# Performance work log

Hardware: AMD Instinct MI355X
Metric: run time of the kernel (lower is better)

Reference implementation:

```python
import jax, jax.numpy as jnp
import numpy as np

B_, L_, H_, P_ = 8, 4096, 512, 256
DT_LO, DT_HI = 1e-3, 4e-3  # keep Heinsen log-space weights in fp32 range for L=4096


def setup_inputs() -> dict:
    key = jax.random.key(0)
    ks = jax.random.split(key, 8)
    u = jax.random.normal(ks[0], (B_, L_, H_), dtype=jnp.float32)
    # Diagonal continuous-time state matrix Lambda (HiPPO-N-like: Re=-0.5, structured imag parts)
    lambda_re = -0.5 * jnp.ones((P_,), dtype=jnp.float32)
    lambda_im = jnp.pi * (jnp.arange(P_, dtype=jnp.float32) + 1.0)
    # Input/output projections (complex, stored as re/im pairs)
    B_re = jax.random.normal(ks[1], (P_, H_), dtype=jnp.float32) / jnp.sqrt(float(H_))
    B_im = jax.random.normal(ks[2], (P_, H_), dtype=jnp.float32) / jnp.sqrt(float(H_))
    C_re = jax.random.normal(ks[3], (H_, P_), dtype=jnp.float32) / jnp.sqrt(float(P_))
    C_im = jax.random.normal(ks[4], (H_, P_), dtype=jnp.float32) / jnp.sqrt(float(P_))
    D = jax.random.normal(ks[5], (H_,), dtype=jnp.float32)
    # Per-state learnable log-timescales, log-uniform in [DT_LO, DT_HI]
    log_delta = jax.random.uniform(ks[6], (P_,), dtype=jnp.float32,
                                   minval=jnp.log(DT_LO), maxval=jnp.log(DT_HI))
    return {"u": u, "lambda_re": lambda_re, "lambda_im": lambda_im,
            "B_re": B_re, "B_im": B_im, "C_re": C_re, "C_im": C_im,
            "D": D, "log_delta": log_delta}


def reference(u, lambda_re, lambda_im, B_re, B_im, C_re, C_im, D, log_delta):
    # --- ZOH discretization (eq. 6 of S5 paper) ---
    lam = lambda_re + 1j * lambda_im                     # (P,) complex64
    delta = jnp.exp(log_delta)                           # (P,)
    lambda_bar = jnp.exp(lam * delta)                    # (P,) complex
    B_tilde = B_re + 1j * B_im                           # (P,H)
    B_bar = ((lambda_bar - 1.0) / lam)[:, None] * B_tilde  # (P,H)

    # --- input projection: Bu_k = B_bar @ u_k ---
    Bu = jnp.einsum('blh,ph->blp', u.astype(B_bar.dtype), B_bar)  # (B,L,P) complex

    # --- Heinsen log-space parallel scan: x_k = lambda_bar * x_{k-1} + Bu_k ---
    L = u.shape[1]
    log_lambda = jnp.log(lambda_bar)                     # (P,) complex
    k = jnp.arange(L, dtype=jnp.float32)
    weights = jnp.exp(k[:, None] * log_lambda[None, :])  # (L,P) complex
    xs = weights[None] * jnp.cumsum(Bu / weights[None], axis=1)  # (B,L,P)

    # --- output: y_k = 2*Re(C_tilde x_k) + D*u_k (conjugate symmetry) ---
    C_tilde = C_re + 1j * C_im                           # (H,P)
    y = 2.0 * jnp.real(jnp.einsum('blp,hp->blh', xs, C_tilde)) + D * u
    return y
```

## Files before the change

kernel.cpp:

```cpp
#include <hip/hip_runtime.h>
#include <hip/hip_bf16.h>
#include <math.h>

#define HH 512
#define PP 256
#define LSEQ 4096
#define BB 8
#define MTOT (BB*LSEQ)
#define N2P 512

typedef __attribute__((ext_vector_type(8))) short bf16x8;
typedef __attribute__((ext_vector_type(4))) float f32x4;
typedef __attribute__((ext_vector_type(8))) unsigned short u16x8;
typedef __attribute__((ext_vector_type(4))) unsigned short u16x4;

#define SWZ(row) (((((row) & 7) ^ (((row) >> 3) & 7)) << 4))

__device__ inline unsigned short f2b(float x) {
    return __builtin_bit_cast(unsigned short, __float2bfloat16(x));
}
__device__ inline float b2f(unsigned short h) {
    union { unsigned int u; float f; } v; v.u = ((unsigned int)h) << 16;
    return v.f;
}

#define GLOAD16(gp, lp) __builtin_amdgcn_global_load_lds( \
    (const __attribute__((address_space(1))) unsigned int*)(gp), \
    (__attribute__((address_space(3))) unsigned int*)(lp), 16, 0, 0)

__device__ inline size_t panel_off(int r, int k) {
    int nblk = r >> 7, rl = r & 127;
    int kblk = k >> 6, kl = k & 63;
    int c = kl >> 3, j = kl & 7;
    return (size_t)(nblk * 8 + kblk) * 16384 + rl * 128 + ((c * 16) ^ SWZ(rl)) + j * 2;
}

__global__ void prep_w1_k(const float* __restrict__ lre, const float* __restrict__ lim,
                          const float* __restrict__ logd,
                          const float* __restrict__ Bre, const float* __restrict__ Bim,
                          char* __restrict__ W1s, float2* __restrict__ lamb) {
    int idx = blockIdx.x * 256 + threadIdx.x;
    if (idx >= PP * HH) return;
    int p = idx >> 9;
    int h = idx & (HH - 1);
    float delta = expf(logd[p]);
    float lr = lre[p], li = lim[p];
    float er = expf(lr * delta);
    float th = li * delta;
    float lbr = er * cosf(th), lbi = er * sinf(th);
    if (h == 0) lamb[p] = make_float2(lbr, lbi);
    float a = lbr - 1.0f, b = lbi;
    float n2 = lr * lr + li * li;
    float gr = (a * lr + b * li) / n2;
    float gi = (b * lr - a * li) / n2;
    float br = Bre[idx], bi = Bim[idx];
    *(unsigned short*)(W1s + panel_off(p, h))      = f2b(gr * br - gi * bi);
    *(unsigned short*)(W1s + panel_off(PP + p, h)) = f2b(gr * bi + gi * br);
}

__global__ void prep_w2_k(const float* __restrict__ Cre, const float* __restrict__ Cim,
                          char* __restrict__ W2s) {
    int idx = blockIdx.x * 256 + threadIdx.x;
    if (idx >= HH * N2P) return;
    int h = idx >> 9;
    int k = idx & 511;
    float v = (k < PP) ? 2.0f * Cre[(size_t)h * PP + k]
                       : -2.0f * Cim[(size_t)h * PP + (k - PP)];
    *(unsigned short*)(W2s + panel_off(h, k)) = f2b(v);
}

__global__ __launch_bounds__(256) void conv_k(const float* __restrict__ u,
                                              char* __restrict__ ub) {
    const int tid = threadIdx.x;
    const int mblk = blockIdx.x >> 2;
    const int sub = blockIdx.x & 3;
    const int ml = sub * 32 + (tid >> 3);
    const int kt = tid & 7;
    const float* src = &u[(size_t)(mblk * 128 + ml) * HH + kt * 64];
    char* dst = ub + ((size_t)(mblk * 8 + kt)) * 16384 + ml * 128;
    #pragma unroll
    for (int c = 0; c < 8; ++c) {
        float4 v0 = *(const float4*)(src + c * 8);
        float4 v1 = *(const float4*)(src + c * 8 + 4);
        bf16x8 pk;
        pk[0] = (short)f2b(v0.x); pk[1] = (short)f2b(v0.y);
        pk[2] = (short)f2b(v0.z); pk[3] = (short)f2b(v0.w);
        pk[4] = (short)f2b(v1.x); pk[5] = (short)f2b(v1.y);
        pk[6] = (short)f2b(v1.z); pk[7] = (short)f2b(v1.w);
        *(bf16x8*)(dst + ((c * 16) ^ SWZ(ml))) = pk;
    }
}

#define TILE_COMPUTE(ABUF, BBUF) { \
    bf16x8 af[4][2], bfv[2][2]; \
    _Pragma("unroll") for (int f = 0; f < 4; ++f) { \
      int ar = wm + f * 16 + (lane & 15); \
      _Pragma("unroll") for (int kk = 0; kk < 2; ++kk) \
        af[f][kk] = *(const bf16x8*)((ABUF) + ar * 128 + ((kk * 64 + (lane >> 4) * 16) ^ SWZ(ar))); } \
    _Pragma("unroll") for (int g = 0; g < 2; ++g) { \
      int br = wn + g * 16 + (lane & 15); \
      _Pragma("unroll") for (int kk = 0; kk < 2; ++kk) \
        bfv[g][kk] = *(const bf16x8*)((BBUF) + br * 128 + ((kk * 64 + (lane >> 4) * 16) ^ SWZ(br))); } \
    _Pragma("unroll") for (int f = 0; f < 4; ++f) \
      _Pragma("unroll") for (int g = 0; g < 2; ++g) \
        _Pragma("unroll") for (int kk = 0; kk < 2; ++kk) \
          acc[f][g] = __builtin_amdgcn_mfma_f32_16x16x32_bf16(af[f][kk], bfv[g][kk], acc[f][g], 0, 0, 0); }

__global__ __launch_bounds__(512, 4) void gemm1_k(const char* __restrict__ ub,
                                                  const char* __restrict__ W1s,
                                                  unsigned short* __restrict__ T1) {
    __shared__ char smem[65536];
    const int tid = threadIdx.x, wave = tid >> 6, lane = tid & 63;
    const int swz = (blockIdx.x & 7) * 128 + (blockIdx.x >> 3);
    const int m0 = (swz >> 2) * 128;
    const int nblk = swz & 3, n0 = nblk * 128;
    const int wm = (wave >> 2) * 64, wn = (wave & 3) * 32;
    const int mblk8 = (m0 >> 7) * 8;

    f32x4 acc[4][2] = {};

#define G1_A_GLOAD(K0, ABUF) { \
    const char* pan = ub + (size_t)(mblk8 + ((K0) >> 6)) * 16384 + tid * 16; \
    GLOAD16(pan, (ABUF) + tid * 16); \
    GLOAD16(pan + 8192, (ABUF) + tid * 16 + 8192); }

#define G1_B_GLOAD(K0, BBUF) { \
    const char* pan = W1s + (size_t)(nblk * 8 + ((K0) >> 6)) * 16384 + tid * 16; \
    GLOAD16(pan, (BBUF) + tid * 16); \
    GLOAD16(pan + 8192, (BBUF) + tid * 16 + 8192); }

    char* A0 = smem;          char* B0 = smem + 16384;
    char* A1 = smem + 32768;  char* B1 = smem + 49152;

    G1_A_GLOAD(0, A0); G1_B_GLOAD(0, B0);

    #pragma unroll
    for (int t = 0; t < 8; ++t) {
        char* Ac = (t & 1) ? A1 : A0; char* Bc = (t & 1) ? B1 : B0;
        char* An = (t & 1) ? A0 : A1; char* Bn = (t & 1) ? B0 : B1;
        if (t < 7) {
            G1_A_GLOAD((t + 1) * 64, An); G1_B_GLOAD((t + 1) * 64, Bn);
            asm volatile("s_waitcnt vmcnt(4)" ::: "memory");
        } else {
            asm volatile("s_waitcnt vmcnt(0)" ::: "memory");
        }
        __syncthreads();
        TILE_COMPUTE(Ac, Bc);
        __syncthreads();
    }

    {
        char* ep = smem;
        #pragma unroll
        for (int f = 0; f < 4; ++f) {
            #pragma unroll
            for (int g = 0; g < 2; ++g) {
                int r = wn + g * 16 + (lane & 15);
                int mb = (wm + f * 16 + ((lane >> 4) << 2)) * 2;
                u16x4 pk;
                pk[0] = f2b(acc[f][g][0]); pk[1] = f2b(acc[f][g][1]);
                pk[2] = f2b(acc[f][g][2]); pk[3] = f2b(acc[f][g][3]);
                *(u16x4*)(ep + r * 256 + (mb ^ ((r & 7) << 4))) = pk;
            }
        }
        __syncthreads();
        #pragma unroll
        for (int it = 0; it < 4; ++it) {
            int r = it * 32 + (tid >> 4);
            int mc = tid & 15;
            u16x8 v = *(const u16x8*)(ep + r * 256 + ((mc * 16) ^ ((r & 7) << 4)));
            *(u16x8*)&T1[(size_t)(n0 + r) * MTOT + m0 + mc * 8] = v;
        }
    }
}

__global__ __launch_bounds__(512, 4) void gemm2_k(const unsigned short* __restrict__ Xs,
                                                  const char* __restrict__ W2s,
                                                  float* __restrict__ y,
                                                  const float* __restrict__ u,
                                                  const float* __restrict__ D) {
    __shared__ char smem[65536];
    const int tid = threadIdx.x, wave = tid >> 6, lane = tid & 63;
    const int swz = (blockIdx.x & 7) * 128 + (blockIdx.x >> 3);
    const int m0 = (swz >> 2) * 128;
    const int nblk = swz & 3, n0 = nblk * 128;
    const int wm = (wave >> 2) * 64, wn = (wave & 3) * 32;
    const int kr = tid >> 5;
    const int mc4 = tid & 31;

    u16x4 xv0[4], xv1[4];
    f32x4 acc[4][2] = {};

#define G2_A_LOAD(SET, K0) { \
    _Pragma("unroll") for (int kk = 0; kk < 4; ++kk) \
        SET[kk] = *(const u16x4*)&Xs[(size_t)((K0) + kr * 4 + kk) * MTOT + m0 + mc4 * 4]; }

#define G2_A_WRITE(SET, ABUF) { \
    _Pragma("unroll") for (int j = 0; j < 4; ++j) { \
        int m = mc4 * 4 + j; \
        u16x4 o; o[0] = SET[0][j]; o[1] = SET[1][j]; o[2] = SET[2][j]; o[3] = SET[3][j]; \
        *(u16x4*)((ABUF) + m * 128 + ((kr * 8) ^ SWZ(m))) = o; } }

#define G2_B_GLOAD(K0, BBUF) { \
    const char* pan = W2s + (size_t)(nblk * 8 + ((K0) >> 6)) * 16384 + tid * 16; \
    GLOAD16(pan, (BBUF) + tid * 16); \
    GLOAD16(pan + 8192, (BBUF) + tid * 16 + 8192); }

    char* A0 = smem;          char* B0 = smem + 16384;
    char* A1 = smem + 32768;  char* B1 = smem + 49152;

    G2_A_LOAD(xv1, 0);
    G2_B_GLOAD(0, B0);
    G2_A_LOAD(xv0, 64);
    asm volatile("s_waitcnt vmcnt(4)" ::: "memory");
    G2_A_WRITE(xv1, A0);
    __syncthreads();

    #pragma unroll
    for (int t = 0; t < 8; ++t) {
        char* Ac = (t & 1) ? A1 : A0; char* Bc = (t & 1) ? B1 : B0;
        char* An = (t & 1) ? A0 : A1; char* Bn = (t & 1) ? B0 : B1;
        if (t < 7) G2_B_GLOAD((t + 1) * 64, Bn);
        if (t < 6) {
            if ((t & 1) == 0) { G2_A_LOAD(xv1, (t + 2) * 64); }
            else              { G2_A_LOAD(xv0, (t + 2) * 64); }
        }
        TILE_COMPUTE(Ac, Bc);
        if (t < 7) {
            if ((t & 1) == 0) { G2_A_WRITE(xv0, An); }
            else              { G2_A_WRITE(xv1, An); }
        }
        if (t < 6)       { asm volatile("s_waitcnt vmcnt(4)" ::: "memory"); }
        else if (t == 6) { asm volatile("s_waitcnt vmcnt(0)" ::: "memory"); }
        __syncthreads();
    }

    float* epi = (float*)smem;
    float* myepi = epi + wave * 2048;
    #pragma unroll
    for (int f = 0; f < 4; ++f) {
        #pragma unroll
        for (int g = 0; g < 2; ++g) {
            int ml = f * 16 + ((lane >> 4) << 2);
            int hl = g * 16 + (lane & 15);
            #pragma unroll
            for (int i = 0; i < 4; ++i)
                myepi[(ml + i) * 32 + hl] = acc[f][g][i];
        }
    }
    __syncthreads();

    #pragma unroll
    for (int it = 0; it < 8; ++it) {
        int idx = it * 512 + tid;
        int ml = idx >> 5, c = idx & 31;
        int w = ((ml >> 6) << 2) + (c >> 3);
        const float4 v = *(const float4*)(epi + w * 2048 + (ml & 63) * 32 + (c & 7) * 4);
        int grow = m0 + ml, gcol = n0 + c * 4;
        const float4 uv = *(const float4*)&u[(size_t)grow * HH + gcol];
        const float4 dv = *(const float4*)&D[gcol];
        float4 o = make_float4(v.x + dv.x * uv.x, v.y + dv.y * uv.y,
                               v.z + dv.z * uv.z, v.w + dv.w * uv.w);
        *(float4*)&y[(size_t)grow * HH + gcol] = o;
    }
}

__global__ __launch_bounds__(256) void scan_k(const unsigned short* __restrict__ T1,
                                              unsigned short* __restrict__ Xs,
                                              const float2* __restrict__ lamb) {
    const int b = blockIdx.x >> 8;
    const int p = blockIdx.x & 255;
    const int t = threadIdx.x;
    const float2 L = lamb[p];

    const size_t baseRe = (size_t)p * MTOT + (size_t)b * LSEQ + t * 16;
    const size_t baseIm = (size_t)(PP + p) * MTOT + (size_t)b * LSEQ + t * 16;

    u16x8 r0 = *(const u16x8*)&T1[baseRe];
    u16x8 r1 = *(const u16x8*)&T1[baseRe + 8];
    u16x8 i0 = *(const u16x8*)&T1[baseIm];
    u16x8 i1 = *(const u16x8*)&T1[baseIm + 8];

    float re[16], im[16];
    #pragma unroll
    for (int j = 0; j < 8; ++j) {
        re[j] = b2f(r0[j]); re[8 + j] = b2f(r1[j]);
        im[j] = b2f(i0[j]); im[8 + j] = b2f(i1[j]);
    }

    float sr = 0.f, si = 0.f;
    #pragma unroll
    for (int j = 0; j < 16; ++j) {
        float nsr = L.x * sr - L.y * si + re[j];
        si = L.x * si + L.y * sr + im[j];
        sr = nsr;
    }

    __shared__ float cr[256], ci[256];
    cr[t] = sr; ci[t] = si;
    __syncthreads();

    float wr = L.x, wi = L.y;
    #pragma unroll
    for (int q = 0; q < 4; ++q) { float nr = wr * wr - wi * wi; wi = 2.f * wr * wi; wr = nr; }

    for (int off = 1; off < 256; off <<= 1) {
        float pr = 0.f, pi = 0.f;
        const bool has = (t >= off);
        if (has) { pr = cr[t - off]; pi = ci[t - off]; }
        __syncthreads();
        if (has) {
            sr += wr * pr - wi * pi;
            si += wr * pi + wi * pr;
            cr[t] = sr; ci[t] = si;
        }
        __syncthreads();
        float nr = wr * wr - wi * wi; wi = 2.f * wr * wi; wr = nr;
    }

    float xr = 0.f, xi = 0.f;
    if (t > 0) { xr = cr[t - 1]; xi = ci[t - 1]; }

    u16x8 o0, o1, o2, o3;
    #pragma unroll
    for (int j = 0; j < 16; ++j) {
        float nr = L.x * xr - L.y * xi + re[j];
        xi = L.x * xi + L.y * xr + im[j];
        xr = nr;
        if (j < 8) { o0[j] = f2b(xr); o2[j] = f2b(xi); }
        else       { o1[j - 8] = f2b(xr); o3[j - 8] = f2b(xi); }
    }
    *(u16x8*)&Xs[baseRe]     = o0;
    *(u16x8*)&Xs[baseRe + 8] = o1;
    *(u16x8*)&Xs[baseIm]     = o2;
    *(u16x8*)&Xs[baseIm + 8] = o3;
}


extern "C" void kernel_launch(void* const* d_in, const int* in_sizes, int n_in,
                              void* d_out, int out_size, void* d_ws, size_t ws_size,
                              hipStream_t stream) {
    const float* u    = (const float*)d_in[0];
    const float* lre  = (const float*)d_in[1];
    const float* lim  = (const float*)d_in[2];
    const float* Bre  = (const float*)d_in[3];
    const float* Bim  = (const float*)d_in[4];
    const float* Cre  = (const float*)d_in[5];
    const float* Cim  = (const float*)d_in[6];
    const float* Dv   = (const float*)d_in[7];
    const float* logd = (const float*)d_in[8];
    float* out = (float*)d_out;

    char* ws = (char*)d_ws;
    char*           W1s  = ws;
    char*           W2s  = ws + (512 << 10);
    float2*         lamb = (float2*)(ws + (1 << 20));
    unsigned short* Xs   = (unsigned short*)(ws + (1 << 20) + 4096);
    char*           ubp  = ws + (1 << 20) + 4096 + ((size_t)32 << 20);

    unsigned short* T1 = (unsigned short*)d_out;

    prep_w1_k<<<(PP * HH) / 256, 256, 0, stream>>>(lre, lim, logd, Bre, Bim, W1s, lamb);
    prep_w2_k<<<(HH * N2P) / 256, 256, 0, stream>>>(Cre, Cim, W2s);

    conv_k<<<1024, 256, 0, stream>>>(u, ubp);
    gemm1_k<<<1024, 512, 0, stream>>>(ubp, W1s, T1);
    scan_k<<<BB * PP, 256, 0, stream>>>(T1, Xs, lamb);
    gemm2_k<<<1024, 512, 0, stream>>>(Xs, W2s, out, u, Dv);
}
```

Measured before the change: 114.4 us.

## Fuse fp32-to-bf16 conversion of u into gemm1 and enlarge per-wave tiles

Removes the separate conversion kernel that wrote a swizzled bf16 copy of u. gemm1 now reads fp32 u directly, converts it in registers and stores it into LDS, which saves one kernel launch and a 32 MB intermediate write and read. gemm1 also moves from 8 waves with 64x32 tiles to 4 waves with 64x64 tiles, using 32 KB of single-buffered LDS. The earlier double-buffered global-to-LDS prefetch is dropped, so loads are no longer overlapped with MFMA compute and each step waits on vmcnt(0) before its barrier.

```diff
diff --git a/kernel.cpp b/kernel.cpp
--- a/kernel.cpp
+++ b/kernel.cpp
@@ -69,25 +69,91 @@
     *(unsigned short*)(W2s + panel_off(h, k)) = f2b(v);
 }
 
-__global__ __launch_bounds__(256) void conv_k(const float* __restrict__ u,
-                                              char* __restrict__ ub) {
-    const int tid = threadIdx.x;
-    const int mblk = blockIdx.x >> 2;
-    const int sub = blockIdx.x & 3;
-    const int ml = sub * 32 + (tid >> 3);
-    const int kt = tid & 7;
-    const float* src = &u[(size_t)(mblk * 128 + ml) * HH + kt * 64];
-    char* dst = ub + ((size_t)(mblk * 8 + kt)) * 16384 + ml * 128;
-    #pragma unroll
-    for (int c = 0; c < 8; ++c) {
-        float4 v0 = *(const float4*)(src + c * 8);
-        float4 v1 = *(const float4*)(src + c * 8 + 4);
-        bf16x8 pk;
-        pk[0] = (short)f2b(v0.x); pk[1] = (short)f2b(v0.y);
-        pk[2] = (short)f2b(v0.z); pk[3] = (short)f2b(v0.w);
-        pk[4] = (short)f2b(v1.x); pk[5] = (short)f2b(v1.y);
-        pk[6] = (short)f2b(v1.z); pk[7] = (short)f2b(v1.w);
-        *(bf16x8*)(dst + ((c * 16) ^ SWZ(ml))) = pk;
+#define TILE_COMPUTE4(ABUF, BBUF) { \
+    bf16x8 af[4][2], bfr[4][2]; \
+    _Pragma("unroll") for (int f = 0; f < 4; ++f) { \
+      _Pragma("unroll") for (int kk = 0; kk < 2; ++kk) { \
+        int ar = wm + f * 16 + (lane & 15); \
+        af[f][kk]  = *(const bf16x8*)((ABUF) + ar * 128 + ((kk * 64 + (lane >> 4) * 16) ^ SWZ(ar))); \
+        int br = wn + f * 16 + (lane & 15); \
+        bfr[f][kk] = *(const bf16x8*)((BBUF) + br * 128 + ((kk * 64 + (lane >> 4) * 16) ^ SWZ(br))); } } \
+    _Pragma("unroll") for (int fm = 0; fm < 4; ++fm) \
+      _Pragma("unroll") for (int fn = 0; fn < 4; ++fn) \
+        _Pragma("unroll") for (int kk = 0; kk < 2; ++kk) \
+          acc[fm][fn] = __builtin_amdgcn_mfma_f32_16x16x32_bf16(af[fm][kk], bfr[fn][kk], acc[fm][fn], 0, 0, 0); }
+
+__global__ __launch_bounds__(256, 4) void gemm1_k(const float* __restrict__ u,
+                                                  const char* __restrict__ W1s,
+                                                  unsigned short* __restrict__ T1) {
+    __shared__ char smem[32768];
+    char* Asw = smem;
+    char* Bsw = smem + 16384;
+    const int tid = threadIdx.x, wave = tid >> 6, lane = tid & 63;
+    const int swz = (blockIdx.x & 7) * 128 + (blockIdx.x >> 3);
+    const int m0 = (swz >> 2) * 128;
+    const int nblk = swz & 3, n0 = nblk * 128;
+    const int wm = (wave >> 1) * 64, wn = (wave & 1) * 64;
+    const int arow = tid >> 1, acol = tid & 1;
+
+    f32x4 acc[4][4] = {};
+
+    for (int t = 0; t < 8; ++t) {
+        const int k0 = t * 64;
+        {
+            const char* pan = W1s + (size_t)(nblk * 8 + t) * 16384 + tid * 16;
+            GLOAD16(pan,         Bsw + tid * 16);
+            GLOAD16(pan + 4096,  Bsw + tid * 16 + 4096);
+            GLOAD16(pan + 8192,  Bsw + tid * 16 + 8192);
+            GLOAD16(pan + 12288, Bsw + tid * 16 + 12288);
+        }
+        #pragma unroll
+        for (int pass = 0; pass < 2; ++pass) {
+            const float* src = &u[(size_t)(m0 + arow) * HH + k0 + acol * 32 + pass * 16];
+            float4 a0 = *(const float4*)(src);
+            float4 a1 = *(const float4*)(src + 4);
+            float4 a2 = *(const float4*)(src + 8);
+            float4 a3 = *(const float4*)(src + 12);
+            bf16x8 p0, p1;
+            p0[0] = (short)f2b(a0.x); p0[1] = (short)f2b(a0.y);
+            p0[2] = (short)f2b(a0.z); p0[3] = (short)f2b(a0.w);
+            p0[4] = (short)f2b(a1.x); p0[5] = (short)f2b(a1.y);
+            p0[6] = (short)f2b(a1.z); p0[7] = (short)f2b(a1.w);
+            p1[0] = (short)f2b(a2.x); p1[1] = (short)f2b(a2.y);
+            p1[2] = (short)f2b(a2.z); p1[3] = (short)f2b(a2.w);
+            p1[4] = (short)f2b(a3.x); p1[5] = (short)f2b(a3.y);
+            p1[6] = (short)f2b(a3.z); p1[7] = (short)f2b(a3.w);
+            int cbase = acol * 64 + pass * 32;
+            *(bf16x8*)(Asw + arow * 128 + ((cbase)      ^ SWZ(arow))) = p0;
+            *(bf16x8*)(Asw + arow * 128 + ((cbase + 16) ^ SWZ(arow))) = p1;
+        }
+        asm volatile("s_waitcnt vmcnt(0)" ::: "memory");
+        __syncthreads();
+        TILE_COMPUTE4(Asw, Bsw);
+        __syncthreads();
+    }
+
+    {
+        char* ep = smem;
+        #pragma unroll
+        for (int fm = 0; fm < 4; ++fm) {
+            #pragma unroll
+            for (int fn = 0; fn < 4; ++fn) {
+                int r = wn + fn * 16 + (lane & 15);
+                int mb = (wm + fm * 16 + ((lane >> 4) << 2)) * 2;
+                u16x4 pk;
+                pk[0] = f2b(acc[fm][fn][0]); pk[1] = f2b(acc[fm][fn][1]);
+                pk[2] = f2b(acc[fm][fn][2]); pk[3] = f2b(acc[fm][fn][3]);
+                *(u16x4*)(ep + r * 256 + (mb ^ ((r & 7) << 4))) = pk;
+            }
+        }
+        __syncthreads();
+        #pragma unroll
+        for (int it = 0; it < 8; ++it) {
+            int idx = it * 256 + tid;
+            int r = idx >> 4, mc = idx & 15;
+            u16x8 v = *(const u16x8*)(ep + r * 256 + ((mc * 16) ^ ((r & 7) << 4)));
+            *(u16x8*)&T1[(size_t)(n0 + r) * MTOT + m0 + mc * 8] = v;
+        }
     }
 }
 
@@ -106,74 +172,6 @@
         _Pragma("unroll") for (int kk = 0; kk < 2; ++kk) \
           acc[f][g] = __builtin_amdgcn_mfma_f32_16x16x32_bf16(af[f][kk], bfv[g][kk], acc[f][g], 0, 0, 0); }
 
-__global__ __launch_bounds__(512, 4) void gemm1_k(const char* __restrict__ ub,
-                                                  const char* __restrict__ W1s,
-                                                  unsigned short* __restrict__ T1) {
-    __shared__ char smem[65536];
-    const int tid = threadIdx.x, wave = tid >> 6, lane = tid & 63;
-    const int swz = (blockIdx.x & 7) * 128 + (blockIdx.x >> 3);
-    const int m0 = (swz >> 2) * 128;
-    const int nblk = swz & 3, n0 = nblk * 128;
-    const int wm = (wave >> 2) * 64, wn = (wave & 3) * 32;
-    const int mblk8 = (m0 >> 7) * 8;
-
-    f32x4 acc[4][2] = {};
-
-#define G1_A_GLOAD(K0, ABUF) { \
-    const char* pan = ub + (size_t)(mblk8 + ((K0) >> 6)) * 16384 + tid * 16; \
-    GLOAD16(pan, (ABUF) + tid * 16); \
-    GLOAD16(pan + 8192, (ABUF) + tid * 16 + 8192); }
-
-#define G1_B_GLOAD(K0, BBUF) { \
-    const char* pan = W1s + (size_t)(nblk * 8 + ((K0) >> 6)) * 16384 + tid * 16; \
-    GLOAD16(pan, (BBUF) + tid * 16); \
-    GLOAD16(pan + 8192, (BBUF) + tid * 16 + 8192); }
-
-    char* A0 = smem;          char* B0 = smem + 16384;
-    char* A1 = smem + 32768;  char* B1 = smem + 49152;
-
-    G1_A_GLOAD(0, A0); G1_B_GLOAD(0, B0);
-
-    #pragma unroll
-    for (int t = 0; t < 8; ++t) {
-        char* Ac = (t & 1) ? A1 : A0; char* Bc = (t & 1) ? B1 : B0;
-        char* An = (t & 1) ? A0 : A1; char* Bn = (t & 1) ? B0 : B1;
-        if (t < 7) {
-            G1_A_GLOAD((t + 1) * 64, An); G1_B_GLOAD((t + 1) * 64, Bn);
-            asm volatile("s_waitcnt vmcnt(4)" ::: "memory");
-        } else {
-            asm volatile("s_waitcnt vmcnt(0)" ::: "memory");
-        }
-        __syncthreads();
-        TILE_COMPUTE(Ac, Bc);
-        __syncthreads();
-    }
-
-    {
-        char* ep = smem;
-        #pragma unroll
-        for (int f = 0; f < 4; ++f) {
-            #pragma unroll
-            for (int g = 0; g < 2; ++g) {
-                int r = wn + g * 16 + (lane & 15);
-                int mb = (wm + f * 16 + ((lane >> 4) << 2)) * 2;
-                u16x4 pk;
-                pk[0] = f2b(acc[f][g][0]); pk[1] = f2b(acc[f][g][1]);
-                pk[2] = f2b(acc[f][g][2]); pk[3] = f2b(acc[f][g][3]);
-                *(u16x4*)(ep + r * 256 + (mb ^ ((r & 7) << 4))) = pk;
-            }
-        }
-        __syncthreads();
-        #pragma unroll
-        for (int it = 0; it < 4; ++it) {
-            int r = it * 32 + (tid >> 4);
-            int mc = tid & 15;
-            u16x8 v = *(const u16x8*)(ep + r * 256 + ((mc * 16) ^ ((r & 7) << 4)));
-            *(u16x8*)&T1[(size_t)(n0 + r) * MTOT + m0 + mc * 8] = v;
-        }
-    }
-}
-
 __global__ __launch_bounds__(512, 4) void gemm2_k(const unsigned short* __restrict__ Xs,
                                                   const char* __restrict__ W2s,
                                                   float* __restrict__ y,
@@ -356,15 +354,13 @@
     char*           W2s  = ws + (512 << 10);
     float2*         lamb = (float2*)(ws + (1 << 20));
     unsigned short* Xs   = (unsigned short*)(ws + (1 << 20) + 4096);
-    char*           ubp  = ws + (1 << 20) + 4096 + ((size_t)32 << 20);
 
     unsigned short* T1 = (unsigned short*)d_out;
 
     prep_w1_k<<<(PP * HH) / 256, 256, 0, stream>>>(lre, lim, logd, Bre, Bim, W1s, lamb);
     prep_w2_k<<<(HH * N2P) / 256, 256, 0, stream>>>(Cre, Cim, W2s);
 
-    conv_k<<<1024, 256, 0, stream>>>(u, ubp);
-    gemm1_k<<<1024, 512, 0, stream>>>(ubp, W1s, T1);
+    gemm1_k<<<1024, 256, 0, stream>>>(u, W1s, T1);
     scan_k<<<BB * PP, 256, 0, stream>>>(T1, Xs, lamb);
     gemm2_k<<<1024, 512, 0, stream>>>(Xs, W2s, out, u, Dv);
 }
```

Measured after the change: 111.1 us. 2.9% less time.

## Fuse fp32-to-bf16 conversion into gemm1 and enlarge its tiles to 256x256

Applied to the files above, without the earlier changes.

Drops the separate conv_k pass. gemm1 now loads fp32 u directly into registers, converts it to bf16 and writes it to swizzled LDS, which removes a full write and re-read of the bf16 copy of u. gemm1 tiles grow from 128x128 to 256x256, with 128KB of LDS and an 8x4 accumulator tile per wave, to get more reuse per load. MFMA sections are wrapped in setprio. The trade-off is lower occupancy, only 256 blocks, and a full vmcnt(0) wait every iteration, so the overlap of loads with compute may be weaker.

```diff
diff --git a/kernel.cpp b/kernel.cpp
--- a/kernel.cpp
+++ b/kernel.cpp
@@ -69,29 +69,102 @@
     *(unsigned short*)(W2s + panel_off(h, k)) = f2b(v);
 }
 
-__global__ __launch_bounds__(256) void conv_k(const float* __restrict__ u,
-                                              char* __restrict__ ub) {
-    const int tid = threadIdx.x;
-    const int mblk = blockIdx.x >> 2;
-    const int sub = blockIdx.x & 3;
-    const int ml = sub * 32 + (tid >> 3);
-    const int kt = tid & 7;
-    const float* src = &u[(size_t)(mblk * 128 + ml) * HH + kt * 64];
-    char* dst = ub + ((size_t)(mblk * 8 + kt)) * 16384 + ml * 128;
-    #pragma unroll
-    for (int c = 0; c < 8; ++c) {
-        float4 v0 = *(const float4*)(src + c * 8);
-        float4 v1 = *(const float4*)(src + c * 8 + 4);
-        bf16x8 pk;
-        pk[0] = (short)f2b(v0.x); pk[1] = (short)f2b(v0.y);
-        pk[2] = (short)f2b(v0.z); pk[3] = (short)f2b(v0.w);
-        pk[4] = (short)f2b(v1.x); pk[5] = (short)f2b(v1.y);
-        pk[6] = (short)f2b(v1.z); pk[7] = (short)f2b(v1.w);
-        *(bf16x8*)(dst + ((c * 16) ^ SWZ(ml))) = pk;
-    }
-}
-
-#define TILE_COMPUTE(ABUF, BBUF) { \
+#define TILE_COMPUTE256(ABUF, BBUF) { \
+    _Pragma("unroll") for (int kk = 0; kk < 2; ++kk) { \
+        bf16x8 af[8], bfv[4]; \
+        _Pragma("unroll") for (int f = 0; f < 8; ++f) { \
+            int ar = wm + f * 16 + (lane & 15); \
+            af[f] = *(const bf16x8*)((ABUF) + ar * 128 + ((kk * 64 + (lane >> 4) * 16) ^ SWZ(ar))); } \
+        _Pragma("unroll") for (int g = 0; g < 4; ++g) { \
+            int br = wn + g * 16 + (lane & 15); \
+            bfv[g] = *(const bf16x8*)((BBUF) + br * 128 + ((kk * 64 + (lane >> 4) * 16) ^ SWZ(br))); } \
+        __builtin_amdgcn_s_setprio(1); \
+        _Pragma("unroll") for (int f = 0; f < 8; ++f) \
+            _Pragma("unroll") for (int g = 0; g < 4; ++g) \
+                acc[f][g] = __builtin_amdgcn_mfma_f32_16x16x32_bf16(af[f], bfv[g], acc[f][g], 0, 0, 0); \
+        __builtin_amdgcn_s_setprio(0); } }
+
+#define B_GLOAD(WS, NB2, K0, BBUF) { \
+    const char* _p0 = (WS) + (size_t)((NB2) * 8 + ((K0) >> 6)) * 16384 + tid * 16; \
+    const char* _p1 = (WS) + (size_t)(((NB2) + 1) * 8 + ((K0) >> 6)) * 16384 + tid * 16; \
+    GLOAD16(_p0, (BBUF) + tid * 16); \
+    GLOAD16(_p0 + 8192, (BBUF) + tid * 16 + 8192); \
+    GLOAD16(_p1, (BBUF) + tid * 16 + 16384); \
+    GLOAD16(_p1 + 8192, (BBUF) + tid * 16 + 24576); }
+
+__global__ __launch_bounds__(512, 2) void gemm1_k(const float* __restrict__ u,
+                                                  const char* __restrict__ W1s,
+                                                  unsigned short* __restrict__ T1) {
+    __shared__ char smem[131072];
+    const int tid = threadIdx.x, wave = tid >> 6, lane = tid & 63;
+    const int swz = (blockIdx.x & 7) * 32 + (blockIdx.x >> 3);
+    const int m0 = (swz >> 1) * 256;
+    const int nb2 = (swz & 1) * 2;
+    const int n0 = (swz & 1) * 256;
+    const int wm = (wave >> 2) * 128, wn = (wave & 3) * 64;
+    const int arow = tid >> 1, ahalf = tid & 1;
+
+    float4 av[8];
+    f32x4 acc[8][4] = {};
+
+#define G1_A_LOAD(K0) { \
+    const float* src = &u[(size_t)(m0 + arow) * HH + (K0) + ahalf * 32]; \
+    _Pragma("unroll") for (int q = 0; q < 8; ++q) av[q] = *(const float4*)(src + q * 4); }
+
+#define G1_A_WRITE(ABUF) { \
+    _Pragma("unroll") for (int c = 0; c < 4; ++c) { \
+        bf16x8 pk; \
+        pk[0] = (short)f2b(av[2*c].x); pk[1] = (short)f2b(av[2*c].y); \
+        pk[2] = (short)f2b(av[2*c].z); pk[3] = (short)f2b(av[2*c].w); \
+        pk[4] = (short)f2b(av[2*c+1].x); pk[5] = (short)f2b(av[2*c+1].y); \
+        pk[6] = (short)f2b(av[2*c+1].z); pk[7] = (short)f2b(av[2*c+1].w); \
+        *(bf16x8*)((ABUF) + arow * 128 + ((ahalf * 64 + c * 16) ^ SWZ(arow))) = pk; } }
+
+    char* A0 = smem;          char* A1 = smem + 32768;
+    char* B0 = smem + 65536;  char* B1 = smem + 98304;
+
+    G1_A_LOAD(0); B_GLOAD(W1s, nb2, 0, B0); G1_A_WRITE(A0);
+    asm volatile("s_waitcnt vmcnt(0)" ::: "memory");
+    __syncthreads();
+
+    #pragma unroll
+    for (int t = 0; t < 8; ++t) {
+        char* Ac = (t & 1) ? A1 : A0; char* Bc = (t & 1) ? B1 : B0;
+        char* An = (t & 1) ? A0 : A1; char* Bn = (t & 1) ? B0 : B1;
+        if (t < 7) { B_GLOAD(W1s, nb2, (t + 1) * 64, Bn); G1_A_LOAD((t + 1) * 64); }
+        TILE_COMPUTE256(Ac, Bc);
+        __builtin_amdgcn_sched_barrier(0);
+        if (t < 7) { G1_A_WRITE(An); }
+        asm volatile("s_waitcnt vmcnt(0)" ::: "memory");
+        __syncthreads();
+    }
+
+    {
+        char* ep = smem;
+        #pragma unroll
+        for (int f = 0; f < 8; ++f) {
+            #pragma unroll
+            for (int g = 0; g < 4; ++g) {
+                int r = wn + g * 16 + (lane & 15);
+                int mb = (wm + f * 16 + ((lane >> 4) << 2)) * 2;
+                u16x4 pk;
+                pk[0] = f2b(acc[f][g][0]); pk[1] = f2b(acc[f][g][1]);
+                pk[2] = f2b(acc[f][g][2]); pk[3] = f2b(acc[f][g][3]);
+                *(u16x4*)(ep + r * 512 + (mb ^ SWZ(r))) = pk;
+            }
+        }
+        __syncthreads();
+        #pragma unroll
+        for (int it = 0; it < 16; ++it) {
+            int idx = it * 512 + tid;
+            int r = idx >> 5, mc = idx & 31;
+            u16x8 v = *(const u16x8*)(ep + r * 512 + ((mc * 16) ^ SWZ(r)));
+            *(u16x8*)&T1[(size_t)(n0 + r) * MTOT + m0 + mc * 8] = v;
+        }
+    }
+}
+
+#define TILE_COMPUTE128(ABUF, BBUF) { \
     bf16x8 af[4][2], bfv[2][2]; \
     _Pragma("unroll") for (int f = 0; f < 4; ++f) { \
       int ar = wm + f * 16 + (lane & 15); \
@@ -106,74 +179,6 @@
         _Pragma("unroll") for (int kk = 0; kk < 2; ++kk) \
           acc[f][g] = __builtin_amdgcn_mfma_f32_16x16x32_bf16(af[f][kk], bfv[g][kk], acc[f][g], 0, 0, 0); }
 
-__global__ __launch_bounds__(512, 4) void gemm1_k(const char* __restrict__ ub,
-                                                  const char* __restrict__ W1s,
-                                                  unsigned short* __restrict__ T1) {
-    __shared__ char smem[65536];
-    const int tid = threadIdx.x, wave = tid >> 6, lane = tid & 63;
-    const int swz = (blockIdx.x & 7) * 128 + (blockIdx.x >> 3);
-    const int m0 = (swz >> 2) * 128;
-    const int nblk = swz & 3, n0 = nblk * 128;
-    const int wm = (wave >> 2) * 64, wn = (wave & 3) * 32;
-    const int mblk8 = (m0 >> 7) * 8;
-
-    f32x4 acc[4][2] = {};
-
-#define G1_A_GLOAD(K0, ABUF) { \
-    const char* pan = ub + (size_t)(mblk8 + ((K0) >> 6)) * 16384 + tid * 16; \
-    GLOAD16(pan, (ABUF) + tid * 16); \
-    GLOAD16(pan + 8192, (ABUF) + tid * 16 + 8192); }
-
-#define G1_B_GLOAD(K0, BBUF) { \
-    const char* pan = W1s + (size_t)(nblk * 8 + ((K0) >> 6)) * 16384 + tid * 16; \
-    GLOAD16(pan, (BBUF) + tid * 16); \
-    GLOAD16(pan + 8192, (BBUF) + tid * 16 + 8192); }
-
-    char* A0 = smem;          char* B0 = smem + 16384;
-    char* A1 = smem + 32768;  char* B1 = smem + 49152;
-
-    G1_A_GLOAD(0, A0); G1_B_GLOAD(0, B0);
-
-    #pragma unroll
-    for (int t = 0; t < 8; ++t) {
-        char* Ac = (t & 1) ? A1 : A0; char* Bc = (t & 1) ? B1 : B0;
-        char* An = (t & 1) ? A0 : A1; char* Bn = (t & 1) ? B0 : B1;
-        if (t < 7) {
-            G1_A_GLOAD((t + 1) * 64, An); G1_B_GLOAD((t + 1) * 64, Bn);
-            asm volatile("s_waitcnt vmcnt(4)" ::: "memory");
-        } else {
-            asm volatile("s_waitcnt vmcnt(0)" ::: "memory");
-        }
-        __syncthreads();
-        TILE_COMPUTE(Ac, Bc);
-        __syncthreads();
-    }
-
-    {
-        char* ep = smem;
-        #pragma unroll
-        for (int f = 0; f < 4; ++f) {
-            #pragma unroll
-            for (int g = 0; g < 2; ++g) {
-                int r = wn + g * 16 + (lane & 15);
-                int mb = (wm + f * 16 + ((lane >> 4) << 2)) * 2;
-                u16x4 pk;
-                pk[0] = f2b(acc[f][g][0]); pk[1] = f2b(acc[f][g][1]);
-                pk[2] = f2b(acc[f][g][2]); pk[3] = f2b(acc[f][g][3]);
-                *(u16x4*)(ep + r * 256 + (mb ^ ((r & 7) << 4))) = pk;
-            }
-        }
-        __syncthreads();
-        #pragma unroll
-        for (int it = 0; it < 4; ++it) {
-            int r = it * 32 + (tid >> 4);
-            int mc = tid & 15;
-            u16x8 v = *(const u16x8*)(ep + r * 256 + ((mc * 16) ^ ((r & 7) << 4)));
-            *(u16x8*)&T1[(size_t)(n0 + r) * MTOT + m0 + mc * 8] = v;
-        }
-    }
-}
-
 __global__ __launch_bounds__(512, 4) void gemm2_k(const unsigned short* __restrict__ Xs,
                                                   const char* __restrict__ W2s,
                                                   float* __restrict__ y,
@@ -225,7 +230,7 @@
             if ((t & 1) == 0) { G2_A_LOAD(xv1, (t + 2) * 64); }
             else              { G2_A_LOAD(xv0, (t + 2) * 64); }
         }
-        TILE_COMPUTE(Ac, Bc);
+        TILE_COMPUTE128(Ac, Bc);
         if (t < 7) {
             if ((t & 1) == 0) { G2_A_WRITE(xv0, An); }
             else              { G2_A_WRITE(xv1, An); }
@@ -356,15 +361,13 @@
     char*           W2s  = ws + (512 << 10);
     float2*         lamb = (float2*)(ws + (1 << 20));
     unsigned short* Xs   = (unsigned short*)(ws + (1 << 20) + 4096);
-    char*           ubp  = ws + (1 << 20) + 4096 + ((size_t)32 << 20);
 
     unsigned short* T1 = (unsigned short*)d_out;
 
     prep_w1_k<<<(PP * HH) / 256, 256, 0, stream>>>(lre, lim, logd, Bre, Bim, W1s, lamb);
     prep_w2_k<<<(HH * N2P) / 256, 256, 0, stream>>>(Cre, Cim, W2s);
 
-    conv_k<<<1024, 256, 0, stream>>>(u, ubp);
-    gemm1_k<<<1024, 512, 0, stream>>>(ubp, W1s, T1);
+    gemm1_k<<<256, 512, 0, stream>>>(u, W1s, T1);
     scan_k<<<BB * PP, 256, 0, stream>>>(T1, Xs, lamb);
     gemm2_k<<<1024, 512, 0, stream>>>(Xs, W2s, out, u, Dv);
 }
```

After: 99.74 us. -12.8%, faster.
